# Kernel tuning notes

Hardware: AMD Instinct MI355X
Metric: run time of the kernel (lower is better)

The kernel has to match this reference:

```python
import jax, jax.numpy as jnp
import numpy as np

B, T, IN, H = 4096, 128, 768, 256


def setup_inputs() -> dict:
    key = jax.random.key(0)
    ks = jax.random.split(key, 5)
    s1 = 1.0 / np.sqrt(IN)
    s2 = 1.0 / np.sqrt(H)
    return {
        "x": jax.random.normal(ks[0], (B, IN), jnp.float32),
        "W1": jax.random.normal(ks[1], (T, IN, H), jnp.float32) * s1,
        "b1": jnp.zeros((T, H), jnp.float32),
        "W2": jax.random.normal(ks[2], (T, H, H), jnp.float32) * s2,
        "b2": jnp.zeros((T, H), jnp.float32),
        "W3": jax.random.normal(ks[3], (T, H), jnp.float32) * s2,
        "b3": jnp.zeros((T,), jnp.float32),
    }


def reference(x, W1, b1, W2, b2, W3, b3):
    # Per-task 3-layer MLP, vectorized over tasks. Dropout is eval-mode (identity).
    h = jax.nn.relu(jnp.einsum('bi,tih->bth', x, W1) + b1)          # [B, T, H]
    h = jax.nn.relu(jnp.einsum('bth,thk->btk', h, W2) + b2)         # [B, T, H]
    out = jnp.einsum('bth,th->bt', h, W3) + b3                      # [B, T]
    return out
```

## Files before the change

### kernel.cpp

```cpp
#include <hip/hip_runtime.h>
#include <cstdint>
#include <cstddef>

#define B_   4096
#define T_   128
#define IN_  768
#define H_   256
#define BM_  128
#define KC1  (IN_ / 32)
#define KC2  (H_ / 32)

typedef __bf16 bf16_t;
typedef bf16_t bf16x8 __attribute__((ext_vector_type(8)));
typedef bf16_t bf16x4 __attribute__((ext_vector_type(4)));
typedef float  floatx16 __attribute__((ext_vector_type(16)));

#define MFMA32(a, b, c) __builtin_amdgcn_mfma_f32_32x32x16_bf16((a), (b), (c), 0, 0, 0)

#define WAITBAR(N) asm volatile("s_waitcnt vmcnt(" #N ") lgkmcnt(0)\n\ts_barrier" ::: "memory")
#define WAIT_LGK_BAR() asm volatile("s_waitcnt lgkmcnt(0)\n\ts_barrier" ::: "memory")

__device__ __forceinline__ void gl_lds16(const bf16_t* g, bf16_t* l) {
    __builtin_amdgcn_global_load_lds(
        (const __attribute__((address_space(1))) void*)g,
        (__attribute__((address_space(3))) void*)l, 16, 0, 0);
}

__device__ __forceinline__ void tile_w_body(const float* __restrict__ src,
                                            bf16_t* __restrict__ dst,
                                            int K, int KC, int blk) {
    const int t  = blk / KC;
    const int kc = blk - t * KC;
    const int kq = threadIdx.x >> 6;
    const int h4 = (threadIdx.x & 63) * 4;
    const float* s = src + ((size_t)t * K + kc * 32 + kq * 8) * H_ + h4;
    float r[8][4];
#pragma unroll
    for (int e = 0; e < 8; ++e) {
        float4 v = *(const float4*)(s + (size_t)e * H_);
        r[e][0] = v.x; r[e][1] = v.y; r[e][2] = v.z; r[e][3] = v.w;
    }
    bf16_t* d = dst + (((size_t)(t * KC + kc) * 4 + kq) * H_ + h4) * 8;
#pragma unroll
    for (int c = 0; c < 4; ++c) {
        bf16x8 v;
#pragma unroll
        for (int e = 0; e < 8; ++e) v[e] = (bf16_t)r[e][c];
        *(bf16x8*)(d + c * 8) = v;
    }
}

__device__ __forceinline__ void tile_x_body(const float* __restrict__ src,
                                            bf16_t* __restrict__ dst, long long o) {
    int m = (int)(o & 127);
    long long q = o >> 7;
    int kq = (int)(q & 3);
    int q2 = (int)(q >> 2);
    int kc   = q2 % KC1;
    int mblk = q2 / KC1;
    const float* s = src + ((long long)mblk * 128 + m) * IN_ + kc * 32 + kq * 8;
    float4 a = *(const float4*)s;
    float4 b = *(const float4*)(s + 4);
    bf16x8 v;
    v[0] = (bf16_t)a.x; v[1] = (bf16_t)a.y; v[2] = (bf16_t)a.z; v[3] = (bf16_t)a.w;
    v[4] = (bf16_t)b.x; v[5] = (bf16_t)b.y; v[6] = (bf16_t)b.z; v[7] = (bf16_t)b.w;
    *(bf16x8*)(dst + o * 8) = v;
}

__global__ __launch_bounds__(256)
void prep_all(const float* __restrict__ x,  bf16_t* __restrict__ xt,
              const float* __restrict__ W1, bf16_t* __restrict__ w1t,
              const float* __restrict__ W2, bf16_t* __restrict__ w2t) {
    const int b = blockIdx.x;
    if (b < 1536) {
        long long o = (long long)b * 256 + threadIdx.x;
        tile_x_body(x, xt, o);
    } else if (b < 1536 + 3072) {
        tile_w_body(W1, w1t, IN_, KC1, b - 1536);
    } else {
        tile_w_body(W2, w2t, H_, KC2, b - 4608);
    }
}

__global__ __launch_bounds__(256, 2)
void mtmlp_fused4(const bf16_t* __restrict__ xt, const bf16_t* __restrict__ w1t,
                  const float* __restrict__ b1, const bf16_t* __restrict__ w2t,
                  const float* __restrict__ b2, const float* __restrict__ W3,
                  const float* __restrict__ b3, float* __restrict__ out) {
    const int L    = blockIdx.x;
    const int xcd  = L & 7;
    const int slot = L >> 3;
    const int t    = xcd * 16 + (slot >> 5);
    const int mblk = slot & 31;
    const int m0   = mblk * BM_;

    const int tid  = threadIdx.x;
    const int lane = tid & 63;
    const int wid  = tid >> 6;
    const int wm   = wid >> 1;
    const int wn   = wid & 1;
    const int ln31 = lane & 31;
    const int hi   = lane >> 5;

    __shared__ __align__(16) bf16_t hbuf[BM_ * H_];
    __shared__ __align__(16) bf16_t wt2[2 * 2 * H_ * 8];
    float* w3s = (float*)wt2;

    floatx16 acc[4][2];
#pragma unroll
    for (int i = 0; i < 4; ++i)
#pragma unroll
        for (int j = 0; j < 2; ++j)
#pragma unroll
            for (int e = 0; e < 16; ++e) acc[i][j][e] = 0.0f;

    const bf16_t* w1base = w1t + (size_t)t * KC1 * 8192;
    const bf16_t* w2base = w2t + (size_t)t * KC2 * 8192;
    const bf16_t* xbase  = xt + (size_t)mblk * KC1 * 4096;

    auto stage1 = [&](bf16_t* buf, int kc) {
        const bf16_t* ws = w1base + (size_t)kc * 8192;
        gl_lds16(ws + tid * 8,        buf + tid * 8);
        gl_lds16(ws + 2048 + tid * 8, buf + 2048 + tid * 8);
        gl_lds16(ws + 4096 + tid * 8, buf + 4096 + tid * 8);
        gl_lds16(ws + 6144 + tid * 8, buf + 6144 + tid * 8);
        const bf16_t* xs = xbase + (size_t)kc * 4096;
        gl_lds16(xs + tid * 8,        buf + 8192 + tid * 8);
        gl_lds16(xs + 2048 + tid * 8, buf + 10240 + tid * 8);
    };
    auto stage2h = [&](bf16_t* dst, int n) {
        const bf16_t* ws = w2base + (size_t)n * 4096;
        gl_lds16(ws + tid * 8,        dst + tid * 8);
        gl_lds16(ws + 2048 + tid * 8, dst + 2048 + tid * 8);
    };
    auto comp1 = [&](const bf16_t* buf) {
#pragma unroll
        for (int s = 0; s < 2; ++s) {
            const int kq = s * 2 + hi;
            bf16x8 A[4], Bf[2];
#pragma unroll
            for (int i = 0; i < 4; ++i)
                A[i] = *(const bf16x8*)(buf + (size_t)(kq * H_ + wm * 128 + i * 32 + ln31) * 8);
#pragma unroll
            for (int j = 0; j < 2; ++j) {
                const int mm = wn * 64 + j * 32 + ln31;
                Bf[j] = *(const bf16x8*)(buf + 8192 + (size_t)(kq * 128 + mm) * 8);
            }
#pragma unroll
            for (int i = 0; i < 4; ++i)
#pragma unroll
                for (int j = 0; j < 2; ++j) acc[i][j] = MFMA32(A[i], Bf[j], acc[i][j]);
        }
    };
    auto comp2 = [&](const bf16_t* wbuf, int n) {
        bf16x8 A[4], Bf[2];
#pragma unroll
        for (int i = 0; i < 4; ++i)
            A[i] = *(const bf16x8*)(wbuf + (size_t)(hi * H_ + wm * 128 + i * 32 + ln31) * 8);
        const int blk = n * 2 + hi;
#pragma unroll
        for (int j = 0; j < 2; ++j) {
            const int mm = wn * 64 + j * 32 + ln31;
            Bf[j] = *(const bf16x8*)(hbuf + (size_t)(blk * BM_ + mm) * 8);
        }
#pragma unroll
        for (int i = 0; i < 4; ++i)
#pragma unroll
            for (int j = 0; j < 2; ++j) acc[i][j] = MFMA32(A[i], Bf[j], acc[i][j]);
    };

    bf16_t* s0 = hbuf;
    bf16_t* s1 = hbuf + 12288;
    stage1(s0, 0);
    stage1(s1, 1);
    for (int p = 0; p < 11; ++p) {
        WAITBAR(6); comp1(s0); WAIT_LGK_BAR(); stage1(s0, 2 * p + 2);
        WAITBAR(6); comp1(s1); WAIT_LGK_BAR(); stage1(s1, 2 * p + 3);
    }
    WAITBAR(6); comp1(s0); WAIT_LGK_BAR(); stage2h(wt2, 0); stage2h(wt2 + 4096, 1);
    WAITBAR(4); comp1(s1); WAIT_LGK_BAR();

#pragma unroll
    for (int i = 0; i < 4; ++i) {
#pragma unroll
        for (int g = 0; g < 4; ++g) {
            const int h0 = wm * 128 + i * 32 + g * 8 + 4 * hi;
            float4 bias = *(const float4*)(b1 + t * H_ + h0);
            const int blk = h0 >> 3;
#pragma unroll
            for (int j = 0; j < 2; ++j) {
                const int mm = wn * 64 + j * 32 + ln31;
                bf16x4 o;
                o[0] = (bf16_t)fmaxf(acc[i][j][4 * g + 0] + bias.x, 0.0f);
                o[1] = (bf16_t)fmaxf(acc[i][j][4 * g + 1] + bias.y, 0.0f);
                o[2] = (bf16_t)fmaxf(acc[i][j][4 * g + 2] + bias.z, 0.0f);
                o[3] = (bf16_t)fmaxf(acc[i][j][4 * g + 3] + bias.w, 0.0f);
                *(bf16x4*)(hbuf + (size_t)(blk * BM_ + mm) * 8 + 4 * hi) = o;
            }
        }
    }

#pragma unroll
    for (int i = 0; i < 4; ++i)
#pragma unroll
        for (int j = 0; j < 2; ++j)
#pragma unroll
            for (int e = 0; e < 16; ++e) acc[i][j][e] = 0.0f;

    for (int np = 0; np < 8; ++np) {
        const int n0 = 2 * np, n1 = 2 * np + 1;
        WAITBAR(2);
        comp2(wt2, n0); WAIT_LGK_BAR();
        if (n0 < 14) stage2h(wt2, n0 + 2);
        if (n1 < 15) { WAITBAR(2); } else { WAITBAR(0); }
        comp2(wt2 + 4096, n1); WAIT_LGK_BAR();
        if (n1 < 14) stage2h(wt2 + 4096, n1 + 2);
    }

    w3s[tid] = W3[t * H_ + tid];
#pragma unroll
    for (int i = 0; i < 4; ++i) {
#pragma unroll
        for (int g = 0; g < 4; ++g) {
            const int h0 = wm * 128 + i * 32 + g * 8 + 4 * hi;
            float4 bias = *(const float4*)(b2 + t * H_ + h0);
            const int blk = h0 >> 3;
#pragma unroll
            for (int j = 0; j < 2; ++j) {
                const int mm = wn * 64 + j * 32 + ln31;
                bf16x4 o;
                o[0] = (bf16_t)fmaxf(acc[i][j][4 * g + 0] + bias.x, 0.0f);
                o[1] = (bf16_t)fmaxf(acc[i][j][4 * g + 1] + bias.y, 0.0f);
                o[2] = (bf16_t)fmaxf(acc[i][j][4 * g + 2] + bias.z, 0.0f);
                o[3] = (bf16_t)fmaxf(acc[i][j][4 * g + 3] + bias.w, 0.0f);
                *(bf16x4*)(hbuf + (size_t)(blk * BM_ + mm) * 8 + 4 * hi) = o;
            }
        }
    }
    WAIT_LGK_BAR();

    {
        const int m = tid >> 1, seg = tid & 1;
        float sum = 0.0f;
#pragma unroll
        for (int b = 0; b < 16; ++b) {
            const int blk = seg * 16 + b;
            const bf16x8 v = *(const bf16x8*)(hbuf + (size_t)(blk * BM_ + m) * 8);
            const float* w = w3s + blk * 8;
#pragma unroll
            for (int e = 0; e < 8; ++e) sum += (float)v[e] * w[e];
        }
        sum += __shfl_xor(sum, 1);
        if (seg == 0) out[(size_t)(m0 + m) * T_ + t] = sum + b3[t];
    }
}

extern "C" void kernel_launch(void* const* d_in, const int* in_sizes, int n_in,
                              void* d_out, int out_size, void* d_ws, size_t ws_size,
                              hipStream_t stream) {
    const float* x  = (const float*)d_in[0];
    const float* W1 = (const float*)d_in[1];
    const float* b1 = (const float*)d_in[2];
    const float* W2 = (const float*)d_in[3];
    const float* b2 = (const float*)d_in[4];
    const float* W3 = (const float*)d_in[5];
    const float* b3 = (const float*)d_in[6];
    float* out = (float*)d_out;

    const size_t nx  = (size_t)B_ * IN_;
    const size_t nw1 = (size_t)T_ * IN_ * H_;

    bf16_t* xt  = (bf16_t*)d_ws;
    bf16_t* w1t = xt + nx;
    bf16_t* w2t = w1t + nw1;

    prep_all<<<dim3(5632), 256, 0, stream>>>(x, xt, W1, w1t, W2, w2t);
    mtmlp_fused4<<<dim3(4096), 256, 0, stream>>>(xt, w1t, b1, w2t, b2, W3, b3, out);
}
```

Baseline: 479.5 us.

## Double row tile to 256 with 512-thread blocks and register-streamed x loads

Doubles the batch tile per block (BM 128→256) using 8 waves, so each staged W1/W2 chunk is reused across twice as many rows and total weight traffic halves. x operands are now loaded straight from global into registers per wave instead of through LDS, and W1 staging uses a 4-slot LDS ring with deeper prefetch. Layer-2 W2 staging is reorganized into full 32-wide k chunks. Risks: hbuf grows to 128KB plus wt2 32KB, so LDS limits occupancy to one block per CU despite launch bounds, and the register-held x loads add VGPR pressure.

```diff
diff --git a/kernel.cpp b/kernel.cpp
--- a/kernel.cpp
+++ b/kernel.cpp
@@ -6,7 +6,7 @@
 #define T_   128
 #define IN_  768
 #define H_   256
-#define BM_  128
+#define BM_  256
 #define KC1  (IN_ / 32)
 #define KC2  (H_ / 32)
 
@@ -82,28 +82,29 @@
     }
 }
 
-__global__ __launch_bounds__(256, 2)
-void mtmlp_fused4(const bf16_t* __restrict__ xt, const bf16_t* __restrict__ w1t,
+__global__ __launch_bounds__(512, 2)
+void mtmlp_fused5(const bf16_t* __restrict__ xt, const bf16_t* __restrict__ w1t,
                   const float* __restrict__ b1, const bf16_t* __restrict__ w2t,
                   const float* __restrict__ b2, const float* __restrict__ W3,
                   const float* __restrict__ b3, float* __restrict__ out) {
     const int L    = blockIdx.x;
     const int xcd  = L & 7;
     const int slot = L >> 3;
-    const int t    = xcd * 16 + (slot >> 5);
-    const int mblk = slot & 31;
+    const int t    = xcd * 16 + (slot >> 4);
+    const int mblk = slot & 15;
     const int m0   = mblk * BM_;
+    const int mb0  = mblk * 2;
 
     const int tid  = threadIdx.x;
     const int lane = tid & 63;
     const int wid  = tid >> 6;
-    const int wm   = wid >> 1;
-    const int wn   = wid & 1;
+    const int wm   = wid >> 2;
+    const int wn   = wid & 3;
     const int ln31 = lane & 31;
     const int hi   = lane >> 5;
 
     __shared__ __align__(16) bf16_t hbuf[BM_ * H_];
-    __shared__ __align__(16) bf16_t wt2[2 * 2 * H_ * 8];
+    __shared__ __align__(16) bf16_t wt2[2 * 4 * H_ * 8];
     float* w3s = (float*)wt2;
 
     floatx16 acc[4][2];
@@ -116,69 +117,85 @@
 
     const bf16_t* w1base = w1t + (size_t)t * KC1 * 8192;
     const bf16_t* w2base = w2t + (size_t)t * KC2 * 8192;
-    const bf16_t* xbase  = xt + (size_t)mblk * KC1 * 4096;
-
-    auto stage1 = [&](bf16_t* buf, int kc) {
+    const bf16_t* xw = xt + (size_t)(mb0 + (wn >> 1)) * KC1 * 4096;
+    const int lbase = hi * 1024 + (wn & 1) * 512 + ln31 * 8;
+    const int abase = hi * 2048 + wm * 1024 + ln31 * 8;
+
+    bf16_t* const sl0 = hbuf;
+    bf16_t* const sl1 = hbuf + 8192;
+    bf16_t* const sl2 = hbuf + 16384;
+    bf16_t* const sl3 = hbuf + 24576;
+
+    auto stageW = [&](bf16_t* dst, int kc) {
         const bf16_t* ws = w1base + (size_t)kc * 8192;
-        gl_lds16(ws + tid * 8,        buf + tid * 8);
-        gl_lds16(ws + 2048 + tid * 8, buf + 2048 + tid * 8);
-        gl_lds16(ws + 4096 + tid * 8, buf + 4096 + tid * 8);
-        gl_lds16(ws + 6144 + tid * 8, buf + 6144 + tid * 8);
-        const bf16_t* xs = xbase + (size_t)kc * 4096;
-        gl_lds16(xs + tid * 8,        buf + 8192 + tid * 8);
-        gl_lds16(xs + 2048 + tid * 8, buf + 10240 + tid * 8);
+        gl_lds16(ws + tid * 8,        dst + tid * 8);
+        gl_lds16(ws + 4096 + tid * 8, dst + 4096 + tid * 8);
     };
-    auto stage2h = [&](bf16_t* dst, int n) {
-        const bf16_t* ws = w2base + (size_t)n * 4096;
+    auto stage2 = [&](bf16_t* dst, int kc) {
+        const bf16_t* ws = w2base + (size_t)kc * 8192;
         gl_lds16(ws + tid * 8,        dst + tid * 8);
-        gl_lds16(ws + 2048 + tid * 8, dst + 2048 + tid * 8);
+        gl_lds16(ws + 4096 + tid * 8, dst + 4096 + tid * 8);
     };
-    auto comp1 = [&](const bf16_t* buf) {
-#pragma unroll
-        for (int s = 0; s < 2; ++s) {
-            const int kq = s * 2 + hi;
-            bf16x8 A[4], Bf[2];
-#pragma unroll
-            for (int i = 0; i < 4; ++i)
-                A[i] = *(const bf16x8*)(buf + (size_t)(kq * H_ + wm * 128 + i * 32 + ln31) * 8);
-#pragma unroll
-            for (int j = 0; j < 2; ++j) {
-                const int mm = wn * 64 + j * 32 + ln31;
-                Bf[j] = *(const bf16x8*)(buf + 8192 + (size_t)(kq * 128 + mm) * 8);
-            }
-#pragma unroll
-            for (int i = 0; i < 4; ++i)
-#pragma unroll
-                for (int j = 0; j < 2; ++j) acc[i][j] = MFMA32(A[i], Bf[j], acc[i][j]);
-        }
-    };
-    auto comp2 = [&](const bf16_t* wbuf, int n) {
-        bf16x8 A[4], Bf[2];
-#pragma unroll
-        for (int i = 0; i < 4; ++i)
-            A[i] = *(const bf16x8*)(wbuf + (size_t)(hi * H_ + wm * 128 + i * 32 + ln31) * 8);
-        const int blk = n * 2 + hi;
-#pragma unroll
-        for (int j = 0; j < 2; ++j) {
-            const int mm = wn * 64 + j * 32 + ln31;
-            Bf[j] = *(const bf16x8*)(hbuf + (size_t)(blk * BM_ + mm) * 8);
-        }
-#pragma unroll
-        for (int i = 0; i < 4; ++i)
-#pragma unroll
-            for (int j = 0; j < 2; ++j) acc[i][j] = MFMA32(A[i], Bf[j], acc[i][j]);
-    };
-
-    bf16_t* s0 = hbuf;
-    bf16_t* s1 = hbuf + 12288;
-    stage1(s0, 0);
-    stage1(s1, 1);
-    for (int p = 0; p < 11; ++p) {
-        WAITBAR(6); comp1(s0); WAIT_LGK_BAR(); stage1(s0, 2 * p + 2);
-        WAITBAR(6); comp1(s1); WAIT_LGK_BAR(); stage1(s1, 2 * p + 3);
-    }
-    WAITBAR(6); comp1(s0); WAIT_LGK_BAR(); stage2h(wt2, 0); stage2h(wt2 + 4096, 1);
-    WAITBAR(4); comp1(s1); WAIT_LGK_BAR();
+
+#define LOADX(XV, kcc) do {                                          \
+        const bf16_t* xp_ = xw + (size_t)(kcc) * 4096;               \
+        XV##0 = *(const bf16x8*)(xp_ + lbase + 0 * 2048 + 0 * 256);  \
+        XV##1 = *(const bf16x8*)(xp_ + lbase + 0 * 2048 + 1 * 256);  \
+        XV##2 = *(const bf16x8*)(xp_ + lbase + 1 * 2048 + 0 * 256);  \
+        XV##3 = *(const bf16x8*)(xp_ + lbase + 1 * 2048 + 1 * 256);  \
+    } while (0)
+
+#define COMP1(bp_, XV) do {                                          \
+        const bf16_t* b_ = (bp_);                                    \
+        bf16x8 A0_, A1_, A2_, A3_;                                   \
+        A0_ = *(const bf16x8*)(b_ + abase + 0 * 4096 + 0 * 256);     \
+        A1_ = *(const bf16x8*)(b_ + abase + 0 * 4096 + 1 * 256);     \
+        A2_ = *(const bf16x8*)(b_ + abase + 0 * 4096 + 2 * 256);     \
+        A3_ = *(const bf16x8*)(b_ + abase + 0 * 4096 + 3 * 256);     \
+        acc[0][0] = MFMA32(A0_, XV##0, acc[0][0]);                   \
+        acc[0][1] = MFMA32(A0_, XV##1, acc[0][1]);                   \
+        acc[1][0] = MFMA32(A1_, XV##0, acc[1][0]);                   \
+        acc[1][1] = MFMA32(A1_, XV##1, acc[1][1]);                   \
+        acc[2][0] = MFMA32(A2_, XV##0, acc[2][0]);                   \
+        acc[2][1] = MFMA32(A2_, XV##1, acc[2][1]);                   \
+        acc[3][0] = MFMA32(A3_, XV##0, acc[3][0]);                   \
+        acc[3][1] = MFMA32(A3_, XV##1, acc[3][1]);                   \
+        A0_ = *(const bf16x8*)(b_ + abase + 1 * 4096 + 0 * 256);     \
+        A1_ = *(const bf16x8*)(b_ + abase + 1 * 4096 + 1 * 256);     \
+        A2_ = *(const bf16x8*)(b_ + abase + 1 * 4096 + 2 * 256);     \
+        A3_ = *(const bf16x8*)(b_ + abase + 1 * 4096 + 3 * 256);     \
+        acc[0][0] = MFMA32(A0_, XV##2, acc[0][0]);                   \
+        acc[0][1] = MFMA32(A0_, XV##3, acc[0][1]);                   \
+        acc[1][0] = MFMA32(A1_, XV##2, acc[1][0]);                   \
+        acc[1][1] = MFMA32(A1_, XV##3, acc[1][1]);                   \
+        acc[2][0] = MFMA32(A2_, XV##2, acc[2][0]);                   \
+        acc[2][1] = MFMA32(A2_, XV##3, acc[2][1]);                   \
+        acc[3][0] = MFMA32(A3_, XV##2, acc[3][0]);                   \
+        acc[3][1] = MFMA32(A3_, XV##3, acc[3][1]);                   \
+    } while (0)
+
+    bf16x8 xA0, xA1, xA2, xA3, xB0, xB1, xB2, xB3;
+
+    stageW(sl0, 0); stageW(sl1, 1); stageW(sl2, 2);
+    LOADX(xA, 0); LOADX(xB, 1);
+
+    WAITBAR(4); stageW(sl3, 3); COMP1(sl0, xA); LOADX(xA, 2);
+    WAITBAR(6); stageW(sl0, 4); COMP1(sl1, xB); LOADX(xB, 3);
+    WAITBAR(6); stageW(sl1, 5); COMP1(sl2, xA); LOADX(xA, 4);
+    WAITBAR(6); stageW(sl2, 6); COMP1(sl3, xB); LOADX(xB, 5);
+
+    for (int q = 1; q <= 4; ++q) {
+        const int kc = q * 4;
+        WAITBAR(6); stageW(sl3, kc + 3); COMP1(sl0, xA); LOADX(xA, kc + 2);
+        WAITBAR(6); stageW(sl0, kc + 4); COMP1(sl1, xB); LOADX(xB, kc + 3);
+        WAITBAR(6); stageW(sl1, kc + 5); COMP1(sl2, xA); LOADX(xA, kc + 4);
+        WAITBAR(6); stageW(sl2, kc + 6); COMP1(sl3, xB); LOADX(xB, kc + 5);
+    }
+    WAITBAR(6); stageW(sl3, 23); COMP1(sl0, xA); LOADX(xA, 22);
+    WAITBAR(6);                  COMP1(sl1, xB); LOADX(xB, 23);
+    WAITBAR(4); stage2(wt2, 0); stage2(wt2 + 8192, 1); COMP1(sl2, xA);
+    WAITBAR(4);                  COMP1(sl3, xB);
+    WAIT_LGK_BAR();
 
 #pragma unroll
     for (int i = 0; i < 4; ++i) {
@@ -207,17 +224,35 @@
 #pragma unroll
             for (int e = 0; e < 16; ++e) acc[i][j][e] = 0.0f;
 
-    for (int np = 0; np < 8; ++np) {
-        const int n0 = 2 * np, n1 = 2 * np + 1;
-        WAITBAR(2);
-        comp2(wt2, n0); WAIT_LGK_BAR();
-        if (n0 < 14) stage2h(wt2, n0 + 2);
-        if (n1 < 15) { WAITBAR(2); } else { WAITBAR(0); }
-        comp2(wt2 + 4096, n1); WAIT_LGK_BAR();
-        if (n1 < 14) stage2h(wt2 + 4096, n1 + 2);
-    }
-
-    w3s[tid] = W3[t * H_ + tid];
+    auto comp2 = [&](const bf16_t* wbuf, int kc) {
+#pragma unroll
+        for (int s = 0; s < 2; ++s) {
+            const int kq = s * 2 + hi;
+            bf16x8 A[4], Bf[2];
+#pragma unroll
+            for (int i = 0; i < 4; ++i)
+                A[i] = *(const bf16x8*)(wbuf + (size_t)(kq * H_ + wm * 128 + i * 32 + ln31) * 8);
+            const int blk = kc * 4 + kq;
+#pragma unroll
+            for (int j = 0; j < 2; ++j) {
+                const int mm = wn * 64 + j * 32 + ln31;
+                Bf[j] = *(const bf16x8*)(hbuf + (size_t)(blk * BM_ + mm) * 8);
+            }
+#pragma unroll
+            for (int i = 0; i < 4; ++i)
+#pragma unroll
+                for (int j = 0; j < 2; ++j) acc[i][j] = MFMA32(A[i], Bf[j], acc[i][j]);
+        }
+    };
+
+    for (int kc = 0; kc < KC2; ++kc) {
+        if (kc < KC2 - 1) { WAITBAR(2); } else { WAITBAR(0); }
+        comp2(wt2 + (kc & 1) * 8192, kc);
+        WAIT_LGK_BAR();
+        if (kc < KC2 - 2) stage2(wt2 + (kc & 1) * 8192, kc + 2);
+    }
+
+    if (tid < H_) w3s[tid] = W3[t * H_ + tid];
 #pragma unroll
     for (int i = 0; i < 4; ++i) {
 #pragma unroll
@@ -253,6 +288,8 @@
         sum += __shfl_xor(sum, 1);
         if (seg == 0) out[(size_t)(m0 + m) * T_ + t] = sum + b3[t];
     }
+#undef LOADX
+#undef COMP1
 }
 
 extern "C" void kernel_launch(void* const* d_in, const int* in_sizes, int n_in,
@@ -275,5 +312,5 @@
     bf16_t* w2t = w1t + nw1;
 
     prep_all<<<dim3(5632), 256, 0, stream>>>(x, xt, W1, w1t, W2, w2t);
-    mtmlp_fused4<<<dim3(4096), 256, 0, stream>>>(xt, w1t, b1, w2t, b2, W3, b3, out);
-}
+    mtmlp_fused5<<<dim3(2048), 512, 0, stream>>>(xt, w1t, b1, w2t, b2, W3, b3, out);
+}
```

Measured after the change: 456.8 us. 1.05x faster.
